# Performance work log

Measured on AMD Instinct MI355X. Metric: run time of the kernel, lower is better.

Reference implementation:

```python
import jax, jax.numpy as jnp
import numpy as np

B, S, D, H, T = 128, 256, 256, 1024, 128  # batch, src_len, input/output_dim, hidden, target_len


def setup_inputs() -> dict:
    key = jax.random.key(0)
    ks = jax.random.split(key, 16)
    sc = 0.05

    def p(k, shape):
        return (jax.random.normal(k, shape, jnp.float32) * sc)

    return {
        "x": jax.random.normal(ks[0], (B, S, D), jnp.float32),
        "x_target": jax.random.normal(ks[1], (B, T, D), jnp.float32),
        # encoder bidirectional LSTM (1 layer): gates order i,f,g,o (PyTorch)
        "enc_Wih_f": p(ks[2], (4 * H, D)),  "enc_Whh_f": p(ks[3], (4 * H, H)), "enc_b_f": p(ks[4], (4 * H,)),
        "enc_Wih_b": p(ks[5], (4 * H, D)),  "enc_Whh_b": p(ks[6], (4 * H, H)), "enc_b_b": p(ks[7], (4 * H,)),
        # decoder bidirectional LSTM (1 layer)
        "dec_Wih_f": p(ks[8], (4 * H, D)),  "dec_Whh_f": p(ks[9], (4 * H, H)), "dec_b_f": p(ks[10], (4 * H,)),
        "dec_Wih_b": p(ks[11], (4 * H, D)), "dec_Whh_b": p(ks[12], (4 * H, H)), "dec_b_b": p(ks[13], (4 * H,)),
        # decoder head: Linear(2H -> D)
        "mlp_W": p(ks[14], (D, 2 * H)), "mlp_b": p(ks[15], (D,)),
    }


def lstm_cell(x, h, c, Wih, Whh, b):
    # x: [B, Din], h/c: [B, H]; PyTorch gate order i, f, g, o
    g = x @ Wih.T + h @ Whh.T + b
    i, f, gg, o = jnp.split(g, 4, axis=-1)
    c = jax.nn.sigmoid(f) * c + jax.nn.sigmoid(i) * jnp.tanh(gg)
    h = jax.nn.sigmoid(o) * jnp.tanh(c)
    return h, c


def run_dir(xs, Wih, Whh, b, reverse):
    # xs: [S, B, Din]; returns final (h, c) for one direction (zero init, like torch LSTM without h0)
    h0 = jnp.zeros((xs.shape[1], Whh.shape[1]), xs.dtype)
    c0 = jnp.zeros_like(h0)

    def step(carry, xt):
        h, c = lstm_cell(xt, *carry, Wih, Whh, b)
        return (h, c), None

    (h, c), _ = jax.lax.scan(step, (h0, c0), xs, reverse=reverse)
    return h, c


def reference(x, x_target, enc_Wih_f, enc_Whh_f, enc_b_f, enc_Wih_b, enc_Whh_b, enc_b_b,
              dec_Wih_f, dec_Whh_f, dec_b_f, dec_Wih_b, dec_Whh_b, dec_b_b, mlp_W, mlp_b):
    xs = jnp.transpose(x, (1, 0, 2))  # [S, B, D], time-major
    hf, cf = run_dir(xs, enc_Wih_f, enc_Whh_f, enc_b_f, reverse=False)
    hb, cb = run_dir(xs, enc_Wih_b, enc_Whh_b, enc_b_b, reverse=True)

    dec_in = x[:, -1, :]  # [B, D]

    def step(carry, _):
        hf, cf, hb, cb, inp = carry
        # bidirectional LSTM on a length-1 sequence: both directions see the same step
        hf2, cf2 = lstm_cell(inp, hf, cf, dec_Wih_f, dec_Whh_f, dec_b_f)
        hb2, cb2 = lstm_cell(inp, hb, cb, dec_Wih_b, dec_Whh_b, dec_b_b)
        out = jnp.concatenate([hf2, hb2], axis=-1) @ mlp_W.T + mlp_b  # [B, D]
        # teacher_forcing_ratio = 0.0 -> always feed model output back
        return (hf2, cf2, hb2, cb2, out), out

    _, outs = jax.lax.scan(step, (hf, cf, hb, cb, dec_in), None, length=T)
    return jnp.transpose(outs, (1, 0, 2))  # [B, T, D]
```

## Files before the change

### kernel.cpp

```cpp
#include <hip/hip_runtime.h>
#include <stdint.h>


typedef __attribute__((ext_vector_type(8))) short bfx8;
typedef __attribute__((ext_vector_type(4))) float f32x4;
typedef __attribute__((ext_vector_type(4))) unsigned short u16x4;
typedef unsigned short ushort_t;
typedef unsigned long long u64;

#define NWG 256
#define MFMA(a,b,c) __builtin_amdgcn_mfma_f32_16x16x32_bf16((a),(b),(c),0,0,0)
#define WAITVM(N) { asm volatile("s_waitcnt vmcnt(" #N ")" ::: "memory"); __builtin_amdgcn_sched_barrier(0); }
#define WAITLG(N) { asm volatile("s_waitcnt lgkmcnt(" #N ")" ::: "memory"); __builtin_amdgcn_sched_barrier(0); }
#define SBAR()    { __builtin_amdgcn_s_barrier(); __builtin_amdgcn_sched_barrier(0); }
#define SCHED0()  __builtin_amdgcn_sched_barrier(0)

__device__ __forceinline__ unsigned short f2bf(float f){
  unsigned u = __float_as_uint(f);
  u += 0x7FFFu + ((u >> 16) & 1u);
  return (unsigned short)(u >> 16);
}
__device__ __forceinline__ float bf2f(unsigned short h){
  return __uint_as_float(((unsigned)h) << 16);
}
__device__ __forceinline__ float sigm(float x){ return 1.f/(1.f + __expf(-x)); }
__device__ __forceinline__ float tanh_(float x){ return 1.f - 2.f/(__expf(2.f*x) + 1.f); }

__device__ __forceinline__ void stage16(const void* g, void* l){
  __builtin_amdgcn_global_load_lds((const __attribute__((address_space(1))) void*)g,
                                   (__attribute__((address_space(3))) void*)l,
                                   16, 0, 0);
}
__device__ __forceinline__ void stage16c(const void* g, void* l){
  __builtin_amdgcn_global_load_lds((const __attribute__((address_space(1))) void*)g,
                                   (__attribute__((address_space(3))) void*)l,
                                   16, 0, 0x11);
}

__device__ __forceinline__ bfx8 ld16c(const ushort_t* p){
  const u64* q = (const u64*)p;
  u64 a = __hip_atomic_load(q,     __ATOMIC_RELAXED, __HIP_MEMORY_SCOPE_AGENT);
  u64 b = __hip_atomic_load(q + 1, __ATOMIC_RELAXED, __HIP_MEMORY_SCOPE_AGENT);
  union { u64 u[2]; bfx8 v; } x; x.u[0] = a; x.u[1] = b; return x.v;
}
__device__ __forceinline__ void sth2(ushort_t* p, unsigned short v){
  __hip_atomic_store(p, v, __ATOMIC_RELAXED, __HIP_MEMORY_SCOPE_AGENT);
}

__device__ __forceinline__ void cvt2(const f32x4& a, const f32x4& b, bfx8& hi, bfx8& lo){
#pragma unroll
  for (int j = 0; j < 4; ++j){
    unsigned short h0 = f2bf(a[j]);
    unsigned short h1 = f2bf(b[j]);
    hi[j]   = (short)h0; lo[j]   = (short)f2bf(a[j] - bf2f(h0));
    hi[4+j] = (short)h1; lo[4+j] = (short)f2bf(b[j] - bf2f(h1));
  }
}

__device__ __forceinline__ void bar(unsigned* flags, int nflags, int me, unsigned gen){
  __syncthreads();
  if (threadIdx.x == 0)
    __hip_atomic_store(&flags[me], gen, __ATOMIC_RELAXED, __HIP_MEMORY_SCOPE_AGENT);
  if (threadIdx.x < 64){
    const int l = threadIdx.x;
    for (;;){
      unsigned mn = 0xFFFFFFFFu;
      for (int o = l; o < nflags; o += 64){
        unsigned v = __hip_atomic_load(&flags[o], __ATOMIC_RELAXED, __HIP_MEMORY_SCOPE_AGENT);
        mn = mn < v ? mn : v;
      }
      if (__all((int)(mn >= gen))) break;
      __builtin_amdgcn_s_sleep(1);
    }
  }
  __syncthreads();
}

struct WPre {
  const ushort_t* pj[8];
  ushort_t* ldsb[2];
  bool active;
};
__device__ __forceinline__ void wpre_issue(const WPre& w){
  if (!w.active) return;
#pragma unroll
  for (int bp = 0; bp < 2; ++bp)
#pragma unroll
    for (int j = 0; j < 8; ++j)
      stage16(w.pj[j] + bp*64, w.ldsb[bp] + j*512);
}
__device__ __forceinline__ void bar_pf(unsigned* flags, int nflags, int me,
                                       unsigned gen, const WPre& w, bool pf){
  WAITLG(0); WAITVM(0);
  SBAR();
  if (pf) wpre_issue(w);
  if (threadIdx.x == 192)
    __hip_atomic_store(&flags[me], gen, __ATOMIC_RELAXED, __HIP_MEMORY_SCOPE_AGENT);
  if ((threadIdx.x >> 6) == 3){
    const int l = threadIdx.x & 63;
    for (;;){
      unsigned mn = 0xFFFFFFFFu;
      for (int o = l; o < nflags; o += 64){
        unsigned v = __hip_atomic_load(&flags[o], __ATOMIC_RELAXED, __HIP_MEMORY_SCOPE_AGENT);
        mn = mn < v ? mn : v;
      }
      if (__all((int)(mn >= gen))) break;
      __builtin_amdgcn_s_sleep(1);
    }
  }
  SBAR();
}

struct Frags { bfx8 awh0, awh1, awl0, awl1, bh0, bh1, bl0, bl1; };

template<int ENC>
__device__ __forceinline__ void cell_step(
    const float*    __restrict__ Wih,
    const ushort_t* __restrict__ WhH,
    const ushort_t* __restrict__ WhL,
    const float*    __restrict__ bias,
    const float*    __restrict__ xsl,
    const ushort_t* __restrict__ iph,
    const ushort_t* __restrict__ ipl,
    const ushort_t* __restrict__ hh,
    const ushort_t* __restrict__ hl,
    ushort_t* __restrict__ outh, ushort_t* __restrict__ outl,
    float (&creg)[2][2],
    int r0, int n0, int b0, ushort_t* LDS)
{
  const int tid  = threadIdx.x;
  const int lane = tid & 63;
  const int wv   = tid >> 6;
  const int wm   = wv >> 1, wn = wv & 1;
  const int lr   = tid >> 3;
  const int lc   = tid & 7;
  const int cb   = lane >> 4;
  const int fr   = lane & 15;
  const int sc8  = lc ^ (lr & 7);
  const int sx   = fr & 7;
  const int rwa0 = wm*32 + fr, rwa1 = rwa0 + 16;
  const int rwb0 = wn*32 + fr, rwb1 = rwb0 + 16;

  const int ra = r0 + lr, rb = ra + 32;
  const float* wih0 = Wih + (size_t)((ra & 3)*1024 + (ra >> 2))*256 + sc8*8;
  const float* wih1 = Wih + (size_t)((rb & 3)*1024 + (rb >> 2))*256 + sc8*8;
  const float *xs0 = nullptr, *xs1 = nullptr;
  const ushort_t *ih0 = nullptr, *ih1 = nullptr, *il0 = nullptr, *il1 = nullptr;
  if (ENC){
    xs0 = xsl + (size_t)(b0 + lr)*65536 + sc8*8;
    xs1 = xs0 + (size_t)32*65536;
  } else {
    ih0 = iph + (size_t)(b0 + lr)*256 + sc8*8;  ih1 = ih0 + 32*256;
    il0 = ipl + (size_t)(b0 + lr)*256 + sc8*8;  il1 = il0 + 32*256;
  }

  const ushort_t* sb; size_t sstr; int srow0;
  if      (wv == 0){ sb = WhH; sstr = 1024; srow0 = r0; }
  else if (wv == 1){ sb = WhL; sstr = 1024; srow0 = r0; }
  else if (wv == 2){ sb = hh;  sstr = 2048; srow0 = b0; }
  else             { sb = hl;  sstr = 2048; srow0 = b0; }
  const int srw = lane >> 3;
  const int sg  = (lane & 7) ^ srw;
  const ushort_t* pj[8];
#pragma unroll
  for (int j = 0; j < 8; ++j)
    pj[j] = sb + (size_t)(srow0 + j*8 + srw)*sstr + sg*8;

  auto ISSUE_W = [&](int c, int s){
    const int ko = (c - 4)*64;
    ushort_t* d = LDS + 16384 + s*8192 + (wv & 1)*4096;
#pragma unroll
    for (int j = 0; j < 8; ++j)
      stage16(pj[j] + ko, d + j*512);
  };
  auto ISSUE_H = [&](int c, int s){
    const int ko = (c - 4)*64;
    ushort_t* d = LDS + 32768 + s*8192 + (wv & 1)*4096;
#pragma unroll
    for (int j = 0; j < 8; ++j)
      stage16c(pj[j] + ko, d + j*512);
  };

  f32x4 acc[2][2] = {};
  auto rdf = [&](const ushort_t* wb, const ushort_t* ab, int ks, Frags& f){
    const int ga = (((ks << 2) + cb) ^ sx) << 3;
    f.awh0 = *(const bfx8*)(wb +        rwa0*64 + ga);
    f.awh1 = *(const bfx8*)(wb +        rwa1*64 + ga);
    f.awl0 = *(const bfx8*)(wb + 4096 + rwa0*64 + ga);
    f.awl1 = *(const bfx8*)(wb + 4096 + rwa1*64 + ga);
    f.bh0  = *(const bfx8*)(ab +        rwb0*64 + ga);
    f.bh1  = *(const bfx8*)(ab +        rwb1*64 + ga);
    f.bl0  = *(const bfx8*)(ab + 4096 + rwb0*64 + ga);
    f.bl1  = *(const bfx8*)(ab + 4096 + rwb1*64 + ga);
  };
  auto mm12 = [&](const Frags& f){
    acc[0][0] = MFMA(f.awh0, f.bh0, acc[0][0]);
    acc[0][0] = MFMA(f.awh0, f.bl0, acc[0][0]);
    acc[0][0] = MFMA(f.awl0, f.bh0, acc[0][0]);
    acc[0][1] = MFMA(f.awh0, f.bh1, acc[0][1]);
    acc[0][1] = MFMA(f.awh0, f.bl1, acc[0][1]);
    acc[0][1] = MFMA(f.awl0, f.bh1, acc[0][1]);
    acc[1][0] = MFMA(f.awh1, f.bh0, acc[1][0]);
    acc[1][0] = MFMA(f.awh1, f.bl0, acc[1][0]);
    acc[1][0] = MFMA(f.awl1, f.bh0, acc[1][0]);
    acc[1][1] = MFMA(f.awh1, f.bh1, acc[1][1]);
    acc[1][1] = MFMA(f.awh1, f.bl1, acc[1][1]);
    acc[1][1] = MFMA(f.awl1, f.bh1, acc[1][1]);
  };

  f32x4 rw[4][4];
  f32x4 rx[4][4];
  bfx8  di[4][4];
#pragma unroll
  for (int c = 0; c < 4; ++c){
    const int kc = c*64;
    rw[c][0] = *(const f32x4*)(wih0 + kc);  rw[c][1] = *(const f32x4*)(wih0 + kc + 4);
    rw[c][2] = *(const f32x4*)(wih1 + kc);  rw[c][3] = *(const f32x4*)(wih1 + kc + 4);
    if (ENC){
      rx[c][0] = *(const f32x4*)(xs0 + kc); rx[c][1] = *(const f32x4*)(xs0 + kc + 4);
      rx[c][2] = *(const f32x4*)(xs1 + kc); rx[c][3] = *(const f32x4*)(xs1 + kc + 4);
    } else {
      di[c][0] = ld16c(ih0 + kc);  di[c][1] = ld16c(ih1 + kc);
      di[c][2] = ld16c(il0 + kc);  di[c][3] = ld16c(il1 + kc);
    }
  }
  SCHED0();
  if (wv >= 2){
#pragma unroll
    for (int s = 0; s < 5; ++s)
      ISSUE_H(4 + s, s);
  }
  SCHED0();
  bfx8 swh[4][2], swl[4][2], sah[4][2], sal[4][2];
#pragma unroll
  for (int c = 0; c < 4; ++c){
    cvt2(rw[c][0], rw[c][1], swh[c][0], swl[c][0]);
    cvt2(rw[c][2], rw[c][3], swh[c][1], swl[c][1]);
    if (ENC){
      cvt2(rx[c][0], rx[c][1], sah[c][0], sal[c][0]);
      cvt2(rx[c][2], rx[c][3], sah[c][1], sal[c][1]);
    } else {
      sah[c][0] = di[c][0]; sah[c][1] = di[c][1];
      sal[c][0] = di[c][2]; sal[c][1] = di[c][3];
    }
  }

#pragma unroll
  for (int c = 0; c < 4; ++c){
    *(bfx8*)(LDS +         lr    *64 + lc*8) = swh[c][0];
    *(bfx8*)(LDS +        (lr+32)*64 + lc*8) = swh[c][1];
    *(bfx8*)(LDS + 4096 +  lr    *64 + lc*8) = swl[c][0];
    *(bfx8*)(LDS + 4096 + (lr+32)*64 + lc*8) = swl[c][1];
    *(bfx8*)(LDS + 8192 +  lr    *64 + lc*8) = sah[c][0];
    *(bfx8*)(LDS + 8192 + (lr+32)*64 + lc*8) = sah[c][1];
    *(bfx8*)(LDS + 12288 + lr    *64 + lc*8) = sal[c][0];
    *(bfx8*)(LDS + 12288 +(lr+32)*64 + lc*8) = sal[c][1];
    WAITLG(0); SBAR();
    Frags f0, f1;
    rdf(LDS, LDS + 8192, 0, f0);
    rdf(LDS, LDS + 8192, 1, f1);
    WAITLG(8);
    mm12(f0);
    WAITLG(0); SBAR();
    mm12(f1);
  }

  int hcs = 0, his = 0;
  for (int i = 4; i <= 19; ++i){
    if (wv < 2){
      if (i <= 18) { WAITVM(8); } else { WAITVM(0); }
    } else {
      if      (i <= 15) { WAITVM(32); }
      else if (i == 16) { WAITVM(24); }
      else if (i == 17) { WAITVM(16); }
      else if (i == 18) { WAITVM(8); }
      else              { WAITVM(0); }
    }
    SBAR();
    const ushort_t* wb = LDS + 16384 + (i & 1)*8192;
    const ushort_t* ab = LDS + 32768 + hcs*8192;
    Frags f0, f1;
    rdf(wb, ab, 0, f0);
    rdf(wb, ab, 1, f1);
    WAITLG(8);
    mm12(f0);
    WAITLG(0); SBAR();
    if (wv < 2){ if (i <= 17) ISSUE_W(i + 2, i & 1); }
    else       { if (i <= 14) ISSUE_H(i + 5, his); }
    mm12(f1);
    hcs = (hcs == 4) ? 0 : hcs + 1;
    his = (his == 4) ? 0 : his + 1;
  }

#pragma unroll
  for (int m = 0; m < 2; ++m){
    const int n = n0 + wm*8 + m*4 + cb;
    const float bi_ = bias[n];
    const float bf_ = bias[1024 + n];
    const float bg_ = bias[2048 + n];
    const float bo_ = bias[3072 + n];
#pragma unroll
    for (int nb = 0; nb < 2; ++nb){
      const int b = b0 + wn*32 + nb*16 + fr;
      float gi = acc[m][nb][0] + bi_;
      float gf = acc[m][nb][1] + bf_;
      float gg = acc[m][nb][2] + bg_;
      float go = acc[m][nb][3] + bo_;
      float c_new = sigm(gf)*creg[m][nb] + sigm(gi)*tanh_(gg);
      float h_new = sigm(go)*tanh_(c_new);
      creg[m][nb] = c_new;
      unsigned short hi = f2bf(h_new);
      sth2(&outh[(size_t)b*2048 + n], hi);
      sth2(&outl[(size_t)b*2048 + n], f2bf(h_new - bf2f(hi)));
    }
  }
}

__device__ __forceinline__ void mlp32(
    const ushort_t* __restrict__ hch, const ushort_t* __restrict__ hcl,
    const ushort_t* __restrict__ mWh, const ushort_t* __restrict__ mWl,
    const float* __restrict__ mb, float* __restrict__ dout,
    ushort_t* __restrict__ inph, ushort_t* __restrict__ inpl,
    int wg, int t, ushort_t* LDS)
{
  const int tid = threadIdx.x, lane = tid & 63, wv = tid >> 6;
  const int d0 = (wg >> 2)*32, b0 = (wg & 3)*32;
  const int kb = wv*512;
  const int srw2 = lane >> 2;
  const int pg   = lane & 3;

  const ushort_t* base[4] = { mWh, mWl, hch, hcl };
  const int rb0[4] = { d0, d0, b0, b0 };
  const ushort_t* sp[8];
#pragma unroll
  for (int j = 0; j < 8; ++j){
    const int p = j >> 1, sub = j & 1;
    const int rl = sub*16 + srw2;
    const int sr = (rl ^ (rl >> 2)) & 3;
    sp[j] = base[p] + (size_t)(rb0[p] + rl)*2048 + kb + ((pg ^ sr)*8);
  }
  ushort_t* lb[4];
#pragma unroll
  for (int s = 0; s < 4; ++s)
    lb[s] = LDS + 8192 + wv*16384 + s*4096;

  auto MISSUE = [&](int c){
    ushort_t* B = lb[c & 3];
    const int ko = c*32;
#pragma unroll
    for (int j = 0; j < 8; ++j){
      const int p = j >> 1, sub = j & 1;
      if (p < 2) stage16 (sp[j] + ko, B + p*1024 + sub*512 + lane*8);
      else       stage16c(sp[j] + ko, B + p*1024 + sub*512 + lane*8);
    }
  };
  MISSUE(0); MISSUE(1); MISSUE(2); MISSUE(3);

  f32x4 acc[2][2] = {};
  const int lg = lane >> 4;
  for (int c = 0; c < 16; ++c){
    if      (c <= 12) { WAITVM(24); }
    else if (c == 13) { WAITVM(16); }
    else if (c == 14) { WAITVM(8); }
    else              { WAITVM(0); }
    const ushort_t* B = lb[c & 3];
    bfx8 wf[2][2], af[2][2];
#pragma unroll
    for (int m = 0; m < 2; ++m){
      const int rl = m*16 + (lane & 15);
      const int sr = (rl ^ (rl >> 2)) & 3;
      const int off = rl*32 + ((lg ^ sr)*8);
      wf[0][m] = *(const bfx8*)(B + off);
      wf[1][m] = *(const bfx8*)(B + 1024 + off);
      af[0][m] = *(const bfx8*)(B + 2048 + off);
      af[1][m] = *(const bfx8*)(B + 3072 + off);
    }
    WAITLG(0);
    if (c < 12) MISSUE(c + 4);
#pragma unroll
    for (int m = 0; m < 2; ++m)
#pragma unroll
      for (int n = 0; n < 2; ++n){
        acc[m][n] = MFMA(wf[0][m], af[0][n], acc[m][n]);
        acc[m][n] = MFMA(wf[0][m], af[1][n], acc[m][n]);
        acc[m][n] = MFMA(wf[1][m], af[0][n], acc[m][n]);
      }
  }

  float* PL = (float*)LDS;
#pragma unroll
  for (int m = 0; m < 2; ++m)
#pragma unroll
    for (int n = 0; n < 2; ++n)
#pragma unroll
      for (int r = 0; r < 4; ++r)
        PL[wv*1024 + (m*2 + n)*256 + r*64 + lane] = acc[m][n][r];
  __syncthreads();
  for (int o = tid; o < 1024; o += 256){
    float s = PL[o] + PL[1024 + o] + PL[2048 + o] + PL[3072 + o];
    const int m = o >> 9, n = (o >> 8) & 1, r = (o >> 6) & 3, l = o & 63;
    const int d = d0 + m*16 + (l >> 4)*4 + r;
    const int b = b0 + n*16 + (l & 15);
    s += mb[d];
    dout[((size_t)b*128 + t)*256 + d] = s;
    const unsigned short hv = f2bf(s);
    sth2(&inph[(size_t)b*256 + d], hv);
    sth2(&inpl[(size_t)b*256 + d], f2bf(s - bf2f(hv)));
  }
}

__device__ __forceinline__ void wg_decode(int wg, int& dir, int& r0, int& n0,
                                          int& b0, int& me){
  const int half = (wg >> 3) & 1;
  const int rgd  = (wg & 7) | ((wg >> 4) << 3);
  dir = rgd >> 6;
  const int rg = rgd & 63;
  r0 = rg * 64; n0 = rg * 16; b0 = half * 64;
  me = (rg << 1) | half;
}

__device__ __forceinline__ WPre make_wpre(const ushort_t* WhH, const ushort_t* WhL,
                                          int r0, ushort_t* LDS){
  const int tid = threadIdx.x, lane = tid & 63, wv = tid >> 6;
  const int srw = lane >> 3;
  const int sg  = (lane & 7) ^ srw;
  WPre w;
  w.active = (wv < 2);
  const ushort_t* sb = (wv == 1) ? WhL : WhH;
#pragma unroll
  for (int j = 0; j < 8; ++j)
    w.pj[j] = sb + (size_t)(r0 + j*8 + srw)*1024 + sg*8;
#pragma unroll
  for (int s = 0; s < 2; ++s)
    w.ldsb[s] = LDS + 16384 + s*8192 + (wv & 1)*4096;
  return w;
}

__global__ void __launch_bounds__(256) rnn_enc_kernel(
    const float* __restrict__ Wih_f, const float* __restrict__ b_f,
    const float* __restrict__ Wih_b, const float* __restrict__ b_b,
    const ushort_t* __restrict__ WhhH, const ushort_t* __restrict__ WhhL,
    const float* __restrict__ x,
    ushort_t* __restrict__ Hh, ushort_t* __restrict__ Hl,
    float* __restrict__ C, unsigned* flagsE)
{
  extern __shared__ ushort_t LDS[];
  int dir, r0, n0, b0, me;
  wg_decode(blockIdx.x, dir, r0, n0, b0, me);
  const float* Wih = dir ? Wih_b : Wih_f;
  const float* bia = dir ? b_b : b_f;
  const ushort_t* WhH = WhhH + (size_t)dir*4096*1024;
  const ushort_t* WhL = WhhL + (size_t)dir*4096*1024;
  unsigned* fl = flagsE + dir*128;
  const WPre wp = make_wpre(WhH, WhL, r0, LDS);

  float creg[2][2] = {{0.f, 0.f}, {0.f, 0.f}};
  wpre_issue(wp);
  for (int t = 0; t < 256; ++t){
    const int tt = dir ? (255 - t) : t;
    const int rp = t & 1;
    cell_step<1>(Wih, WhH, WhL, bia,
                 x + (size_t)tt*256, nullptr, nullptr,
                 Hh + (size_t)rp     *262144 + dir*1024,
                 Hl + (size_t)rp     *262144 + dir*1024,
                 Hh + (size_t)(rp^1) *262144 + dir*1024,
                 Hl + (size_t)(rp^1) *262144 + dir*1024,
                 creg, r0, n0, b0, LDS);
    bar_pf(fl, 128, me, (unsigned)(t + 1), wp, t < 255);
  }
  {
    const int lane = threadIdx.x & 63, wv = threadIdx.x >> 6;
    const int wm = wv >> 1, wn = wv & 1, cb = lane >> 4, fr = lane & 15;
    float* Cst = C + (size_t)dir*1024*128;
#pragma unroll
    for (int m = 0; m < 2; ++m)
#pragma unroll
      for (int nb = 0; nb < 2; ++nb){
        const int n = n0 + wm*8 + m*4 + cb;
        const int b = b0 + wn*32 + nb*16 + fr;
        Cst[n*128 + b] = creg[m][nb];
      }
  }
}

__global__ void __launch_bounds__(256) rnn_dec_kernel(
    const float* __restrict__ Wih_f, const float* __restrict__ b_f,
    const float* __restrict__ Wih_b, const float* __restrict__ b_b,
    const ushort_t* __restrict__ WhhH, const ushort_t* __restrict__ WhhL,
    const ushort_t* __restrict__ mWh, const ushort_t* __restrict__ mWl,
    const float* __restrict__ mb,
    ushort_t* __restrict__ Hh, ushort_t* __restrict__ Hl,
    float* __restrict__ C,
    ushort_t* __restrict__ inph, ushort_t* __restrict__ inpl,
    float* __restrict__ dout, unsigned* flagsD)
{
  extern __shared__ ushort_t LDS[];
  const int wg = blockIdx.x;
  int dir, r0, n0, b0, me;
  wg_decode(wg, dir, r0, n0, b0, me);
  const float* Wih = dir ? Wih_b : Wih_f;
  const float* bia = dir ? b_b : b_f;
  const ushort_t* WhH = WhhH + (size_t)dir*4096*1024;
  const ushort_t* WhL = WhhL + (size_t)dir*4096*1024;
  const WPre wp = make_wpre(WhH, WhL, r0, LDS);

  float creg[2][2];
  {
    const int lane = threadIdx.x & 63, wv = threadIdx.x >> 6;
    const int wm = wv >> 1, wn = wv & 1, cb = lane >> 4, fr = lane & 15;
    const float* Cst = C + (size_t)dir*1024*128;
#pragma unroll
    for (int m = 0; m < 2; ++m)
#pragma unroll
      for (int nb = 0; nb < 2; ++nb){
        const int n = n0 + wm*8 + m*4 + cb;
        const int b = b0 + wn*32 + nb*16 + fr;
        creg[m][nb] = Cst[n*128 + b];
      }
  }
  wpre_issue(wp);
  for (int t = 0; t < 128; ++t){
    const int rp = t & 1;
    cell_step<0>(Wih, WhH, WhL, bia,
                 nullptr, inph, inpl,
                 Hh + (size_t)rp     *262144 + dir*1024,
                 Hl + (size_t)rp     *262144 + dir*1024,
                 Hh + (size_t)(rp^1) *262144 + dir*1024,
                 Hl + (size_t)(rp^1) *262144 + dir*1024,
                 creg, r0, n0, b0, LDS);
    bar(flagsD, 256, wg, (unsigned)(2*t + 1));
    if (wg < 32)
      mlp32(Hh + (size_t)(rp^1)*262144, Hl + (size_t)(rp^1)*262144,
            mWh, mWl, mb, dout, inph, inpl, wg, t, LDS);
    bar_pf(flagsD, 256, wg, (unsigned)(2*t + 2), wp, t < 127);
  }
}

__global__ void k_wplanes(ushort_t* Hp, ushort_t* Lp,
                          const float* Whh_f, const float* Whh_b)
{
  const size_t N = 2ull*4096*1024;
  for (size_t i = (size_t)blockIdx.x*blockDim.x + threadIdx.x; i < N;
       i += (size_t)gridDim.x*blockDim.x){
    int dir = (int)(i >> 22);
    int r   = (int)((i >> 10) & 4095);
    int k   = (int)(i & 1023);
    int n = r >> 2, q = r & 3;
    const float* W = dir ? Whh_b : Whh_f;
    float v = W[(size_t)(q*1024 + n)*1024 + k];
    unsigned short h = f2bf(v);
    Hp[i] = h;
    Lp[i] = f2bf(v - bf2f(h));
  }
}

__global__ void k_init(ushort_t* Hh, ushort_t* Hl,
                       ushort_t* inph, ushort_t* inpl,
                       ushort_t* mWh, ushort_t* mWl,
                       const float* x, const float* mW, unsigned* cnt)
{
  const size_t N = 524288;
  for (size_t i = (size_t)blockIdx.x*blockDim.x + threadIdx.x; i < N;
       i += (size_t)gridDim.x*blockDim.x){
    Hh[i] = 0; Hl[i] = 0;
    float wv = mW[i];
    unsigned short wh = f2bf(wv);
    mWh[i] = wh;
    mWl[i] = f2bf(wv - bf2f(wh));
    if (i < 32768){
      int b = (int)(i >> 8), d = (int)(i & 255);
      float v = x[((size_t)b*256 + 255)*256 + d];
      unsigned short hi = f2bf(v);
      inph[i] = hi;
      inpl[i] = f2bf(v - bf2f(hi));
    }
    if (i < 2048) cnt[i] = 0;
  }
}

extern "C" void kernel_launch(void* const* d_in, const int* in_sizes, int n_in,
                              void* d_out, int out_size, void* d_ws, size_t ws_size,
                              hipStream_t stream)
{
  (void)in_sizes; (void)n_in; (void)out_size; (void)ws_size;
  const float* x      = (const float*)d_in[0];
  const float* eWih_f = (const float*)d_in[2];
  const float* eWhh_f = (const float*)d_in[3];
  const float* eb_f   = (const float*)d_in[4];
  const float* eWih_b = (const float*)d_in[5];
  const float* eWhh_b = (const float*)d_in[6];
  const float* eb_b   = (const float*)d_in[7];
  const float* dWih_f = (const float*)d_in[8];
  const float* dWhh_f = (const float*)d_in[9];
  const float* db_f   = (const float*)d_in[10];
  const float* dWih_b = (const float*)d_in[11];
  const float* dWhh_b = (const float*)d_in[12];
  const float* db_b   = (const float*)d_in[13];
  const float* mW     = (const float*)d_in[14];
  const float* mb     = (const float*)d_in[15];

  char* p = (char*)d_ws;
  size_t off = 0;
  unsigned* cnt   = (unsigned*)(p + off);  off += 8192;
  ushort_t* WhhEh = (ushort_t*)(p + off);  off += 16777216;
  ushort_t* WhhEl = (ushort_t*)(p + off);  off += 16777216;
  ushort_t* WhhDh = (ushort_t*)(p + off);  off += 16777216;
  ushort_t* WhhDl = (ushort_t*)(p + off);  off += 16777216;
  ushort_t* mWh   = (ushort_t*)(p + off);  off += 1048576;
  ushort_t* mWl   = (ushort_t*)(p + off);  off += 1048576;
  ushort_t* Hh    = (ushort_t*)(p + off);  off += 1048576;
  ushort_t* Hl    = (ushort_t*)(p + off);  off += 1048576;
  float*    C     = (float*)(p + off);     off += 1048576;
  ushort_t* inph  = (ushort_t*)(p + off);  off += 65536;
  ushort_t* inpl  = (ushort_t*)(p + off);  off += 65536;

  unsigned* flagsD = cnt;
  unsigned* flagsE = cnt + 256;

  hipFuncSetAttribute(reinterpret_cast<const void*>(rnn_enc_kernel),
                      hipFuncAttributeMaxDynamicSharedMemorySize, 147456);
  hipFuncSetAttribute(reinterpret_cast<const void*>(rnn_dec_kernel),
                      hipFuncAttributeMaxDynamicSharedMemorySize, 147456);

  k_init   <<<512, 256, 0, stream>>>(Hh, Hl, inph, inpl, mWh, mWl, x, mW, cnt);
  k_wplanes<<<2048, 256, 0, stream>>>(WhhEh, WhhEl, eWhh_f, eWhh_b);
  k_wplanes<<<2048, 256, 0, stream>>>(WhhDh, WhhDl, dWhh_f, dWhh_b);

  rnn_enc_kernel<<<NWG, 256, 147456, stream>>>(eWih_f, eb_f, eWih_b, eb_b,
                                               WhhEh, WhhEl, x, Hh, Hl, C, flagsE);
  rnn_dec_kernel<<<NWG, 256, 147456, stream>>>(dWih_f, db_f, dWih_b, db_b,
                                               WhhDh, WhhDl, mWh, mWl, mb,
                                               Hh, Hl, C, inph, inpl,
                                               (float*)d_out, flagsD);
}
```

Before: 10.44 ms.

## Retile LSTM cell to 128-row x 32-batch tiles with async LDS staging of Wih/x

Changes each workgroup's tile from 64 gate rows by 64 batch to 128 gate rows by 32 batch. Waves 0-1 now stream weights and waves 2-3 stream activations. The input-projection weights and x/decoder input are no longer loaded into registers, converted and written to LDS by hand; they are staged asynchronously into LDS with global_load_lds and split into hi/lo bf16 at fragment-read time. The whole 20-chunk K loop becomes a single pipelined schedule with explicit vmcnt waits. The goal is to overlap input-projection loads with compute and reuse activations across more gate rows, at the cost of reloading the weight tile per batch quarter and a more intricate wait-count schedule.

```diff
diff --git a/kernel.cpp b/kernel.cpp
--- a/kernel.cpp
+++ b/kernel.cpp
@@ -13,7 +13,6 @@
 #define WAITVM(N) { asm volatile("s_waitcnt vmcnt(" #N ")" ::: "memory"); __builtin_amdgcn_sched_barrier(0); }
 #define WAITLG(N) { asm volatile("s_waitcnt lgkmcnt(" #N ")" ::: "memory"); __builtin_amdgcn_sched_barrier(0); }
 #define SBAR()    { __builtin_amdgcn_s_barrier(); __builtin_amdgcn_sched_barrier(0); }
-#define SCHED0()  __builtin_amdgcn_sched_barrier(0)
 
 __device__ __forceinline__ unsigned short f2bf(float f){
   unsigned u = __float_as_uint(f);
@@ -35,13 +34,6 @@
   __builtin_amdgcn_global_load_lds((const __attribute__((address_space(1))) void*)g,
                                    (__attribute__((address_space(3))) void*)l,
                                    16, 0, 0x11);
-}
-
-__device__ __forceinline__ bfx8 ld16c(const ushort_t* p){
-  const u64* q = (const u64*)p;
-  u64 a = __hip_atomic_load(q,     __ATOMIC_RELAXED, __HIP_MEMORY_SCOPE_AGENT);
-  u64 b = __hip_atomic_load(q + 1, __ATOMIC_RELAXED, __HIP_MEMORY_SCOPE_AGENT);
-  union { u64 u[2]; bfx8 v; } x; x.u[0] = a; x.u[1] = b; return x.v;
 }
 __device__ __forceinline__ void sth2(ushort_t* p, unsigned short v){
   __hip_atomic_store(p, v, __ATOMIC_RELAXED, __HIP_MEMORY_SCOPE_AGENT);
@@ -55,6 +47,81 @@
     hi[j]   = (short)h0; lo[j]   = (short)f2bf(a[j] - bf2f(h0));
     hi[4+j] = (short)h1; lo[4+j] = (short)f2bf(b[j] - bf2f(h1));
   }
+}
+
+template<int ENC>
+struct Stg {
+  const float*    wih;
+  const ushort_t* whhb;
+  const float*    xb;
+  const ushort_t* ipb;
+  const ushort_t* hb;
+  int wdst, adst, r0;
+  int lane, wv;
+
+  __device__ void issue_w(int c, ushort_t* LDS) const {
+    if (wv >= 2) return;
+    ushort_t* d = LDS + (c & 1)*16384 + wdst;
+    if (c < 4){
+#pragma unroll
+      for (int j = 0; j < 16; ++j){
+        const int rp_ = r0 + (wv & 1)*64 + j*4 + (lane >> 4);
+        const int srcrow = ((rp_ & 3) << 10) + (rp_ >> 2);
+        stage16(wih + (size_t)srcrow*256 + (lane & 15)*4 + c*64, d + j*512);
+      }
+    } else {
+#pragma unroll
+      for (int j = 0; j < 16; ++j)
+        stage16(whhb + j*8192 + (c - 4)*64, d + j*512);
+    }
+  }
+  __device__ void issue_a(int c, int slot, ushort_t* LDS,
+                          int xoff, unsigned hoff) const {
+    if (wv < 2) return;
+    ushort_t* d = LDS + 32768 + slot*4096 + adst;
+    if (c < 4){
+      if (ENC){
+#pragma unroll
+        for (int j = 0; j < 4; ++j)
+          stage16(xb + (size_t)j*262144 + xoff + c*64, d + j*512);
+      } else {
+#pragma unroll
+        for (int j = 0; j < 4; ++j)
+          stage16c(ipb + j*2048 + c*64, d + j*512);
+      }
+    } else {
+#pragma unroll
+      for (int j = 0; j < 4; ++j)
+        stage16c(hb + (size_t)j*16384 + hoff + (c - 4)*64, d + j*512);
+    }
+  }
+};
+
+template<int ENC>
+__device__ __forceinline__ Stg<ENC> make_stg(
+    const float* Wih, const ushort_t* WhH, const ushort_t* WhL,
+    const float* x, const ushort_t* inph, const ushort_t* inpl,
+    const ushort_t* Hhd, const ushort_t* Hld,
+    int r0, int b0)
+{
+  const int lane = threadIdx.x & 63;
+  const int wv   = threadIdx.x >> 6;
+  const int srw  = lane >> 3;
+  const int sg   = (lane & 7) ^ srw;
+  Stg<ENC> s;
+  s.wih = Wih; s.r0 = r0; s.lane = lane; s.wv = wv;
+  s.wdst = (wv & 1)*8192;
+  s.adst = (wv == 3) ? 2048 : 0;
+  s.whhb = ((wv == 1) ? WhL : WhH) + (size_t)(r0 + srw)*1024 + sg*8;
+  if (ENC){
+    s.xb  = x + (size_t)(b0 + ((wv == 3) ? 16 : 0) + (lane >> 4))*65536 + (lane & 15)*4;
+    s.ipb = nullptr;
+  } else {
+    s.xb  = nullptr;
+    s.ipb = ((wv == 3) ? inpl : inph) + (size_t)(b0 + srw)*256 + sg*8;
+  }
+  s.hb = ((wv == 3) ? Hld : Hhd) + (size_t)(b0 + srw)*2048 + sg*8;
+  return s;
 }
 
 __device__ __forceinline__ void bar(unsigned* flags, int nflags, int me, unsigned gen){
@@ -76,24 +143,20 @@
   __syncthreads();
 }
 
-struct WPre {
-  const ushort_t* pj[8];
-  ushort_t* ldsb[2];
-  bool active;
-};
-__device__ __forceinline__ void wpre_issue(const WPre& w){
-  if (!w.active) return;
-#pragma unroll
-  for (int bp = 0; bp < 2; ++bp)
-#pragma unroll
-    for (int j = 0; j < 8; ++j)
-      stage16(w.pj[j] + bp*64, w.ldsb[bp] + j*512);
-}
+template<int ENC>
 __device__ __forceinline__ void bar_pf(unsigned* flags, int nflags, int me,
-                                       unsigned gen, const WPre& w, bool pf){
+                                       unsigned gen, const Stg<ENC>& sg_,
+                                       ushort_t* LDS, bool pf, int xoffn){
   WAITLG(0); WAITVM(0);
   SBAR();
-  if (pf) wpre_issue(w);
+  if (pf){
+    if ((threadIdx.x >> 6) < 2){
+      sg_.issue_w(0, LDS); sg_.issue_w(1, LDS);
+    } else if (ENC){
+#pragma unroll
+      for (int c = 0; c < 4; ++c) sg_.issue_a(c, c, LDS, xoffn, 0);
+    }
+  }
   if (threadIdx.x == 192)
     __hip_atomic_store(&flags[me], gen, __ATOMIC_RELAXED, __HIP_MEMORY_SCOPE_AGENT);
   if ((threadIdx.x >> 6) == 3){
@@ -115,83 +178,37 @@
 
 template<int ENC>
 __device__ __forceinline__ void cell_step(
-    const float*    __restrict__ Wih,
-    const ushort_t* __restrict__ WhH,
-    const ushort_t* __restrict__ WhL,
-    const float*    __restrict__ bias,
-    const float*    __restrict__ xsl,
-    const ushort_t* __restrict__ iph,
-    const ushort_t* __restrict__ ipl,
-    const ushort_t* __restrict__ hh,
-    const ushort_t* __restrict__ hl,
+    const Stg<ENC>& sg_, const float* __restrict__ bias,
     ushort_t* __restrict__ outh, ushort_t* __restrict__ outl,
-    float (&creg)[2][2],
-    int r0, int n0, int b0, ushort_t* LDS)
-{
-  const int tid  = threadIdx.x;
-  const int lane = tid & 63;
-  const int wv   = tid >> 6;
-  const int wm   = wv >> 1, wn = wv & 1;
-  const int lr   = tid >> 3;
-  const int lc   = tid & 7;
+    float (&creg)[2][2], unsigned hoff,
+    int n0, int b0, ushort_t* LDS)
+{
+  const int lane = threadIdx.x & 63;
+  const int wv   = threadIdx.x >> 6;
   const int cb   = lane >> 4;
   const int fr   = lane & 15;
-  const int sc8  = lc ^ (lr & 7);
   const int sx   = fr & 7;
-  const int rwa0 = wm*32 + fr, rwa1 = rwa0 + 16;
-  const int rwb0 = wn*32 + fr, rwb1 = rwb0 + 16;
-
-  const int ra = r0 + lr, rb = ra + 32;
-  const float* wih0 = Wih + (size_t)((ra & 3)*1024 + (ra >> 2))*256 + sc8*8;
-  const float* wih1 = Wih + (size_t)((rb & 3)*1024 + (rb >> 2))*256 + sc8*8;
-  const float *xs0 = nullptr, *xs1 = nullptr;
-  const ushort_t *ih0 = nullptr, *ih1 = nullptr, *il0 = nullptr, *il1 = nullptr;
-  if (ENC){
-    xs0 = xsl + (size_t)(b0 + lr)*65536 + sc8*8;
-    xs1 = xs0 + (size_t)32*65536;
-  } else {
-    ih0 = iph + (size_t)(b0 + lr)*256 + sc8*8;  ih1 = ih0 + 32*256;
-    il0 = ipl + (size_t)(b0 + lr)*256 + sc8*8;  il1 = il0 + 32*256;
-  }
-
-  const ushort_t* sb; size_t sstr; int srow0;
-  if      (wv == 0){ sb = WhH; sstr = 1024; srow0 = r0; }
-  else if (wv == 1){ sb = WhL; sstr = 1024; srow0 = r0; }
-  else if (wv == 2){ sb = hh;  sstr = 2048; srow0 = b0; }
-  else             { sb = hl;  sstr = 2048; srow0 = b0; }
-  const int srw = lane >> 3;
-  const int sg  = (lane & 7) ^ srw;
-  const ushort_t* pj[8];
-#pragma unroll
-  for (int j = 0; j < 8; ++j)
-    pj[j] = sb + (size_t)(srow0 + j*8 + srw)*sstr + sg*8;
-
-  auto ISSUE_W = [&](int c, int s){
-    const int ko = (c - 4)*64;
-    ushort_t* d = LDS + 16384 + s*8192 + (wv & 1)*4096;
-#pragma unroll
-    for (int j = 0; j < 8; ++j)
-      stage16(pj[j] + ko, d + j*512);
-  };
-  auto ISSUE_H = [&](int c, int s){
-    const int ko = (c - 4)*64;
-    ushort_t* d = LDS + 32768 + s*8192 + (wv & 1)*4096;
-#pragma unroll
-    for (int j = 0; j < 8; ++j)
-      stage16c(pj[j] + ko, d + j*512);
-  };
+  const int rwa0 = wv*32 + fr, rwa1 = rwa0 + 16;
+  const int rwb0 = fr, rwb1 = fr + 16;
+
+  if (!ENC){
+#pragma unroll
+    for (int c = 0; c < 4; ++c) sg_.issue_a(c, c, LDS, 0, hoff);
+  }
+#pragma unroll
+  for (int c = 4; c < 9; ++c) sg_.issue_a(c, c, LDS, 0, hoff);
 
   f32x4 acc[2][2] = {};
   auto rdf = [&](const ushort_t* wb, const ushort_t* ab, int ks, Frags& f){
     const int ga = (((ks << 2) + cb) ^ sx) << 3;
     f.awh0 = *(const bfx8*)(wb +        rwa0*64 + ga);
     f.awh1 = *(const bfx8*)(wb +        rwa1*64 + ga);
-    f.awl0 = *(const bfx8*)(wb + 4096 + rwa0*64 + ga);
-    f.awl1 = *(const bfx8*)(wb + 4096 + rwa1*64 + ga);
+    f.awl0 = *(const bfx8*)(wb + 8192 + rwa0*64 + ga);
+    f.awl1 = *(const bfx8*)(wb + 8192 + rwa1*64 + ga);
     f.bh0  = *(const bfx8*)(ab +        rwb0*64 + ga);
     f.bh1  = *(const bfx8*)(ab +        rwb1*64 + ga);
-    f.bl0  = *(const bfx8*)(ab + 4096 + rwb0*64 + ga);
-    f.bl1  = *(const bfx8*)(ab + 4096 + rwb1*64 + ga);
+    f.bl0  = *(const bfx8*)(ab + 2048 + rwb0*64 + ga);
+    f.bl1  = *(const bfx8*)(ab + 2048 + rwb1*64 + ga);
   };
   auto mm12 = [&](const Frags& f){
     acc[0][0] = MFMA(f.awh0, f.bh0, acc[0][0]);
@@ -208,100 +225,106 @@
     acc[1][1] = MFMA(f.awl1, f.bh1, acc[1][1]);
   };
 
-  f32x4 rw[4][4];
-  f32x4 rx[4][4];
-  bfx8  di[4][4];
-#pragma unroll
-  for (int c = 0; c < 4; ++c){
-    const int kc = c*64;
-    rw[c][0] = *(const f32x4*)(wih0 + kc);  rw[c][1] = *(const f32x4*)(wih0 + kc + 4);
-    rw[c][2] = *(const f32x4*)(wih1 + kc);  rw[c][3] = *(const f32x4*)(wih1 + kc + 4);
-    if (ENC){
-      rx[c][0] = *(const f32x4*)(xs0 + kc); rx[c][1] = *(const f32x4*)(xs0 + kc + 4);
-      rx[c][2] = *(const f32x4*)(xs1 + kc); rx[c][3] = *(const f32x4*)(xs1 + kc + 4);
+  int as = 0;
+  for (int i = 0; i < 20; ++i){
+    if (wv < 2){
+      if (i <= 18)      { WAITVM(16); }
+      else              { WAITVM(0); }
     } else {
-      di[c][0] = ld16c(ih0 + kc);  di[c][1] = ld16c(ih1 + kc);
-      di[c][2] = ld16c(il0 + kc);  di[c][3] = ld16c(il1 + kc);
-    }
-  }
-  SCHED0();
-  if (wv >= 2){
-#pragma unroll
-    for (int s = 0; s < 5; ++s)
-      ISSUE_H(4 + s, s);
-  }
-  SCHED0();
-  bfx8 swh[4][2], swl[4][2], sah[4][2], sal[4][2];
-#pragma unroll
-  for (int c = 0; c < 4; ++c){
-    cvt2(rw[c][0], rw[c][1], swh[c][0], swl[c][0]);
-    cvt2(rw[c][2], rw[c][3], swh[c][1], swl[c][1]);
-    if (ENC){
-      cvt2(rx[c][0], rx[c][1], sah[c][0], sal[c][0]);
-      cvt2(rx[c][2], rx[c][3], sah[c][1], sal[c][1]);
+      if      (i <= 11) { WAITVM(32); }
+      else if (i == 12) { WAITVM(28); }
+      else if (i == 13) { WAITVM(24); }
+      else if (i == 14) { WAITVM(20); }
+      else if (i == 15) { WAITVM(16); }
+      else if (i == 16) { WAITVM(12); }
+      else if (i == 17) { WAITVM(8); }
+      else if (i == 18) { WAITVM(4); }
+      else              { WAITVM(0); }
+    }
+    SBAR();
+    const ushort_t* wb = LDS + (i & 1)*16384;
+    const ushort_t* ab = LDS + 32768 + as*4096;
+
+    if (i < 4){
+      const float* wf = (const float*)wb;
+      const int ka0 = cb*8, ka1 = (4 + cb)*8;
+      f32x4 w0a, w0b, w1a, w1b, w2a, w2b, w3a, w3b;
+      f32x4 x0a, x0b, x1a, x1b, x2a, x2b, x3a, x3b;
+      bfx8 dh0, dl0, dh1, dl1, dh2, dl2, dh3, dl3;
+      w0a = *(const f32x4*)(wf + rwa0*64 + ka0);
+      w0b = *(const f32x4*)(wf + rwa0*64 + ka0 + 4);
+      w1a = *(const f32x4*)(wf + rwa1*64 + ka0);
+      w1b = *(const f32x4*)(wf + rwa1*64 + ka0 + 4);
+      if (ENC){
+        const float* af = (const float*)ab;
+        x0a = *(const f32x4*)(af + rwb0*64 + ka0);
+        x0b = *(const f32x4*)(af + rwb0*64 + ka0 + 4);
+        x1a = *(const f32x4*)(af + rwb1*64 + ka0);
+        x1b = *(const f32x4*)(af + rwb1*64 + ka0 + 4);
+      } else {
+        const int ga0 = (cb ^ sx) << 3;
+        dh0 = *(const bfx8*)(ab +        rwb0*64 + ga0);
+        dl0 = *(const bfx8*)(ab + 2048 + rwb0*64 + ga0);
+        dh1 = *(const bfx8*)(ab +        rwb1*64 + ga0);
+        dl1 = *(const bfx8*)(ab + 2048 + rwb1*64 + ga0);
+      }
+      w2a = *(const f32x4*)(wf + rwa0*64 + ka1);
+      w2b = *(const f32x4*)(wf + rwa0*64 + ka1 + 4);
+      w3a = *(const f32x4*)(wf + rwa1*64 + ka1);
+      w3b = *(const f32x4*)(wf + rwa1*64 + ka1 + 4);
+      if (ENC){
+        const float* af = (const float*)ab;
+        x2a = *(const f32x4*)(af + rwb0*64 + ka1);
+        x2b = *(const f32x4*)(af + rwb0*64 + ka1 + 4);
+        x3a = *(const f32x4*)(af + rwb1*64 + ka1);
+        x3b = *(const f32x4*)(af + rwb1*64 + ka1 + 4);
+      } else {
+        const int ga1 = ((4 + cb) ^ sx) << 3;
+        dh2 = *(const bfx8*)(ab +        rwb0*64 + ga1);
+        dl2 = *(const bfx8*)(ab + 2048 + rwb0*64 + ga1);
+        dh3 = *(const bfx8*)(ab +        rwb1*64 + ga1);
+        dl3 = *(const bfx8*)(ab + 2048 + rwb1*64 + ga1);
+      }
+      WAITLG(8);
+      Frags f0;
+      cvt2(w0a, w0b, f0.awh0, f0.awl0);
+      cvt2(w1a, w1b, f0.awh1, f0.awl1);
+      if (ENC){ cvt2(x0a, x0b, f0.bh0, f0.bl0); cvt2(x1a, x1b, f0.bh1, f0.bl1); }
+      else    { f0.bh0 = dh0; f0.bl0 = dl0; f0.bh1 = dh1; f0.bl1 = dl1; }
+      mm12(f0);
+      WAITLG(0); SBAR();
+      if (wv < 2) sg_.issue_w(i + 2, LDS);
+      else        sg_.issue_a(i + 9, as, LDS, 0, hoff);
+      Frags f1;
+      cvt2(w2a, w2b, f1.awh0, f1.awl0);
+      cvt2(w3a, w3b, f1.awh1, f1.awl1);
+      if (ENC){ cvt2(x2a, x2b, f1.bh0, f1.bl0); cvt2(x3a, x3b, f1.bh1, f1.bl1); }
+      else    { f1.bh0 = dh2; f1.bl0 = dl2; f1.bh1 = dh3; f1.bl1 = dl3; }
+      mm12(f1);
     } else {
-      sah[c][0] = di[c][0]; sah[c][1] = di[c][1];
-      sal[c][0] = di[c][2]; sal[c][1] = di[c][3];
-    }
-  }
-
-#pragma unroll
-  for (int c = 0; c < 4; ++c){
-    *(bfx8*)(LDS +         lr    *64 + lc*8) = swh[c][0];
-    *(bfx8*)(LDS +        (lr+32)*64 + lc*8) = swh[c][1];
-    *(bfx8*)(LDS + 4096 +  lr    *64 + lc*8) = swl[c][0];
-    *(bfx8*)(LDS + 4096 + (lr+32)*64 + lc*8) = swl[c][1];
-    *(bfx8*)(LDS + 8192 +  lr    *64 + lc*8) = sah[c][0];
-    *(bfx8*)(LDS + 8192 + (lr+32)*64 + lc*8) = sah[c][1];
-    *(bfx8*)(LDS + 12288 + lr    *64 + lc*8) = sal[c][0];
-    *(bfx8*)(LDS + 12288 +(lr+32)*64 + lc*8) = sal[c][1];
-    WAITLG(0); SBAR();
-    Frags f0, f1;
-    rdf(LDS, LDS + 8192, 0, f0);
-    rdf(LDS, LDS + 8192, 1, f1);
-    WAITLG(8);
-    mm12(f0);
-    WAITLG(0); SBAR();
-    mm12(f1);
-  }
-
-  int hcs = 0, his = 0;
-  for (int i = 4; i <= 19; ++i){
-    if (wv < 2){
-      if (i <= 18) { WAITVM(8); } else { WAITVM(0); }
-    } else {
-      if      (i <= 15) { WAITVM(32); }
-      else if (i == 16) { WAITVM(24); }
-      else if (i == 17) { WAITVM(16); }
-      else if (i == 18) { WAITVM(8); }
-      else              { WAITVM(0); }
-    }
-    SBAR();
-    const ushort_t* wb = LDS + 16384 + (i & 1)*8192;
-    const ushort_t* ab = LDS + 32768 + hcs*8192;
-    Frags f0, f1;
-    rdf(wb, ab, 0, f0);
-    rdf(wb, ab, 1, f1);
-    WAITLG(8);
-    mm12(f0);
-    WAITLG(0); SBAR();
-    if (wv < 2){ if (i <= 17) ISSUE_W(i + 2, i & 1); }
-    else       { if (i <= 14) ISSUE_H(i + 5, his); }
-    mm12(f1);
-    hcs = (hcs == 4) ? 0 : hcs + 1;
-    his = (his == 4) ? 0 : his + 1;
+      Frags f0, f1;
+      rdf(wb, ab, 0, f0);
+      rdf(wb, ab, 1, f1);
+      WAITLG(8);
+      mm12(f0);
+      WAITLG(0); SBAR();
+      if (wv < 2){ if (i <= 17) sg_.issue_w(i + 2, LDS); }
+      else       { if (i <= 10) sg_.issue_a(i + 9, as, LDS, 0, hoff); }
+      mm12(f1);
+    }
+    as = (as == 8) ? 0 : as + 1;
   }
 
 #pragma unroll
   for (int m = 0; m < 2; ++m){
-    const int n = n0 + wm*8 + m*4 + cb;
+    const int n = n0 + wv*8 + m*4 + cb;
     const float bi_ = bias[n];
     const float bf_ = bias[1024 + n];
     const float bg_ = bias[2048 + n];
     const float bo_ = bias[3072 + n];
 #pragma unroll
     for (int nb = 0; nb < 2; ++nb){
-      const int b = b0 + wn*32 + nb*16 + fr;
+      const int b = b0 + nb*16 + fr;
       float gi = acc[m][nb][0] + bi_;
       float gf = acc[m][nb][1] + bf_;
       float gg = acc[m][nb][2] + bg_;
@@ -411,29 +434,14 @@
 
 __device__ __forceinline__ void wg_decode(int wg, int& dir, int& r0, int& n0,
                                           int& b0, int& me){
-  const int half = (wg >> 3) & 1;
-  const int rgd  = (wg & 7) | ((wg >> 4) << 3);
-  dir = rgd >> 6;
-  const int rg = rgd & 63;
-  r0 = rg * 64; n0 = rg * 16; b0 = half * 64;
-  me = (rg << 1) | half;
-}
-
-__device__ __forceinline__ WPre make_wpre(const ushort_t* WhH, const ushort_t* WhL,
-                                          int r0, ushort_t* LDS){
-  const int tid = threadIdx.x, lane = tid & 63, wv = tid >> 6;
-  const int srw = lane >> 3;
-  const int sg  = (lane & 7) ^ srw;
-  WPre w;
-  w.active = (wv < 2);
-  const ushort_t* sb = (wv == 1) ? WhL : WhH;
-#pragma unroll
-  for (int j = 0; j < 8; ++j)
-    w.pj[j] = sb + (size_t)(r0 + j*8 + srw)*1024 + sg*8;
-#pragma unroll
-  for (int s = 0; s < 2; ++s)
-    w.ldsb[s] = LDS + 16384 + s*8192 + (wv & 1)*4096;
-  return w;
+  const int slot = wg & 7;
+  const int rest = wg >> 3;
+  const int q    = rest & 3;
+  const int rgd  = slot | ((rest >> 2) << 3);
+  dir = rgd >> 5;
+  const int rg = rgd & 31;
+  r0 = rg * 128; n0 = rg * 32; b0 = q * 32;
+  me = ((rgd & 31) << 2) | q;
 }
 
 __global__ void __launch_bounds__(256) rnn_enc_kernel(
@@ -452,32 +460,39 @@
   const ushort_t* WhH = WhhH + (size_t)dir*4096*1024;
   const ushort_t* WhL = WhhL + (size_t)dir*4096*1024;
   unsigned* fl = flagsE + dir*128;
-  const WPre wp = make_wpre(WhH, WhL, r0, LDS);
+  const Stg<1> sg_ = make_stg<1>(Wih, WhH, WhL, x, nullptr, nullptr,
+                                 Hh + dir*1024, Hl + dir*1024, r0, b0);
 
   float creg[2][2] = {{0.f, 0.f}, {0.f, 0.f}};
-  wpre_issue(wp);
+  {
+    const int wv = threadIdx.x >> 6;
+    const int xoff0 = (dir ? 255 : 0) * 256;
+    if (wv < 2){ sg_.issue_w(0, LDS); sg_.issue_w(1, LDS); }
+    else {
+#pragma unroll
+      for (int c = 0; c < 4; ++c) sg_.issue_a(c, c, LDS, xoff0, 0);
+    }
+  }
   for (int t = 0; t < 256; ++t){
-    const int tt = dir ? (255 - t) : t;
     const int rp = t & 1;
-    cell_step<1>(Wih, WhH, WhL, bia,
-                 x + (size_t)tt*256, nullptr, nullptr,
-                 Hh + (size_t)rp     *262144 + dir*1024,
-                 Hl + (size_t)rp     *262144 + dir*1024,
-                 Hh + (size_t)(rp^1) *262144 + dir*1024,
-                 Hl + (size_t)(rp^1) *262144 + dir*1024,
-                 creg, r0, n0, b0, LDS);
-    bar_pf(fl, 128, me, (unsigned)(t + 1), wp, t < 255);
+    cell_step<1>(sg_, bia,
+                 Hh + (size_t)(rp^1)*262144 + dir*1024,
+                 Hl + (size_t)(rp^1)*262144 + dir*1024,
+                 creg, (unsigned)rp*262144u, n0, b0, LDS);
+    const bool pf = (t < 255);
+    const int ttn = dir ? (255 - (t + 1)) : (t + 1);
+    bar_pf<1>(fl, 128, me, (unsigned)(t + 1), sg_, LDS, pf, pf ? ttn*256 : 0);
   }
   {
     const int lane = threadIdx.x & 63, wv = threadIdx.x >> 6;
-    const int wm = wv >> 1, wn = wv & 1, cb = lane >> 4, fr = lane & 15;
+    const int cb = lane >> 4, fr = lane & 15;
     float* Cst = C + (size_t)dir*1024*128;
 #pragma unroll
     for (int m = 0; m < 2; ++m)
 #pragma unroll
       for (int nb = 0; nb < 2; ++nb){
-        const int n = n0 + wm*8 + m*4 + cb;
-        const int b = b0 + wn*32 + nb*16 + fr;
+        const int n = n0 + wv*8 + m*4 + cb;
+        const int b = b0 + nb*16 + fr;
         Cst[n*128 + b] = creg[m][nb];
       }
   }
@@ -502,37 +517,35 @@
   const float* bia = dir ? b_b : b_f;
   const ushort_t* WhH = WhhH + (size_t)dir*4096*1024;
   const ushort_t* WhL = WhhL + (size_t)dir*4096*1024;
-  const WPre wp = make_wpre(WhH, WhL, r0, LDS);
+  const Stg<0> sg_ = make_stg<0>(Wih, WhH, WhL, nullptr, inph, inpl,
+                                 Hh + dir*1024, Hl + dir*1024, r0, b0);
 
   float creg[2][2];
   {
     const int lane = threadIdx.x & 63, wv = threadIdx.x >> 6;
-    const int wm = wv >> 1, wn = wv & 1, cb = lane >> 4, fr = lane & 15;
+    const int cb = lane >> 4, fr = lane & 15;
     const float* Cst = C + (size_t)dir*1024*128;
 #pragma unroll
     for (int m = 0; m < 2; ++m)
 #pragma unroll
       for (int nb = 0; nb < 2; ++nb){
-        const int n = n0 + wm*8 + m*4 + cb;
-        const int b = b0 + wn*32 + nb*16 + fr;
+        const int n = n0 + wv*8 + m*4 + cb;
+        const int b = b0 + nb*16 + fr;
         creg[m][nb] = Cst[n*128 + b];
       }
   }
-  wpre_issue(wp);
+  if ((threadIdx.x >> 6) < 2){ sg_.issue_w(0, LDS); sg_.issue_w(1, LDS); }
   for (int t = 0; t < 128; ++t){
     const int rp = t & 1;
-    cell_step<0>(Wih, WhH, WhL, bia,
-                 nullptr, inph, inpl,
-                 Hh + (size_t)rp     *262144 + dir*1024,
-                 Hl + (size_t)rp     *262144 + dir*1024,
-                 Hh + (size_t)(rp^1) *262144 + dir*1024,
-                 Hl + (size_t)(rp^1) *262144 + dir*1024,
-                 creg, r0, n0, b0, LDS);
+    cell_step<0>(sg_, bia,
+                 Hh + (size_t)(rp^1)*262144 + dir*1024,
+                 Hl + (size_t)(rp^1)*262144 + dir*1024,
+                 creg, (unsigned)rp*262144u, n0, b0, LDS);
     bar(flagsD, 256, wg, (unsigned)(2*t + 1));
     if (wg < 32)
       mlp32(Hh + (size_t)(rp^1)*262144, Hl + (size_t)(rp^1)*262144,
             mWh, mWl, mb, dout, inph, inpl, wg, t, LDS);
-    bar_pf(flagsD, 256, wg, (unsigned)(2*t + 2), wp, t < 127);
+    bar_pf<0>(flagsD, 256, wg, (unsigned)(2*t + 2), sg_, LDS, t < 127, 0);
   }
 }
 
```

Result: slower. 12.73 ms (+21.8%).
